# Performance work log

Hardware: AMD Instinct MI355X
Metric: run time of the kernel (lower is better)

## Reference

```python
import jax, jax.numpy as jnp
import numpy as np

EMA = 0.999
EPS = 1e-8


def setup_inputs() -> dict:
    key = jax.random.key(0)
    k1, k2, k3 = jax.random.split(key, 3)
    B, z_dim, H, W = 16, 64, 32, 32
    M = 4096
    N = B * H * W
    return {
        "z": jax.random.normal(k1, (B, z_dim, H, W), dtype=jnp.float32),
        "e": jax.random.normal(k2, (M, z_dim), dtype=jnp.float32),
        "belong": jax.random.uniform(k3, (N, M), dtype=jnp.float32),
        "log_sigma": jnp.zeros((1,), dtype=jnp.float32),
        "max_distance": jnp.ones((1, M), dtype=jnp.float32),
        "distance_p": 2,
    }


def reference(z, e, belong, log_sigma, max_distance, distance_p):
    B, z_dim, H, W = z.shape
    # [B, z_dim, H, W] -> [N, z_dim], N = B*H*W
    zf = jnp.transpose(z, (0, 2, 3, 1)).reshape(-1, z_dim)
    # pairwise L2 distance via GEMM expansion: ||z||^2 + ||e||^2 - 2 z.e
    d2 = (jnp.sum(zf * zf, axis=1, keepdims=True)
          + jnp.sum(e * e, axis=1)[None, :]
          - 2.0 * (zf @ e.T))                      # [N, M]
    distance = jnp.sqrt(jnp.maximum(d2, 0.0))
    # EMA update of per-code max distance (buffer, no grad in original)
    batch_max = jnp.max(belong * distance, axis=0, keepdims=True)  # [1, M]
    new_max = EMA * max_distance + (1.0 - EMA) * batch_max
    new_max = jax.lax.stop_gradient(jnp.clip(new_max, EPS, None))
    p = float(distance_p)
    distance = jnp.where(distance < new_max,
                         distance ** (2.0 / p),
                         distance ** (2.0 * p))
    alpha = -1.0 / (2.0 * jnp.exp(log_sigma) ** 2)  # shape (1,)
    lse = jax.scipy.special.logsumexp(alpha * distance, axis=0)  # [M]
    loss = -jnp.mean(lse) + z_dim * log_sigma  # shape (1,), as in torch
    return loss
```

## Files before the change

### kernel.cpp

```cpp
#include <hip/hip_runtime.h>
#include <hip/hip_bf16.h>

#define ZD   64
#define MM   4096
#define NN   16384
#define HWSZ 1024
#define BB   16

typedef __bf16 bf16x8 __attribute__((ext_vector_type(8)));
typedef float  f32x4  __attribute__((ext_vector_type(4)));

#define EMA_C 0.999f
#define EPS_C 1e-8f

__global__ __launch_bounds__(256) void k_prep(const float* __restrict__ z,
                                              const float* __restrict__ e,
                                              __hip_bfloat16* __restrict__ zf,
                                              __hip_bfloat16* __restrict__ ebf,
                                              float* __restrict__ zn2,
                                              float* __restrict__ en2,
                                              unsigned* __restrict__ bmax,
                                              unsigned* __restrict__ dmin,
                                              float* __restrict__ sume) {
    __shared__ float tile[64][65];
    __shared__ float part[4][64];
    int blk = blockIdx.x;
    int tid = threadIdx.x;
    if (blk < 256) {
        int b   = blk >> 4;
        int hw0 = (blk & 15) * 64;
        int tx = tid & 63, ty = tid >> 6;
        const float* zp = z + (size_t)b * (ZD * HWSZ);
#pragma unroll
        for (int kk = 0; kk < 16; kk++) {
            int k = kk * 4 + ty;
            tile[k][tx] = zp[(size_t)k * HWSZ + hw0 + tx];
        }
        __syncthreads();
#pragma unroll
        for (int i = 0; i < 16; i++) {
            int li = tid + i * 256;
            int ln = li >> 6, lk = li & 63;
            int n = b * HWSZ + hw0 + ln;
            zf[(size_t)n * ZD + lk] = __float2bfloat16(tile[lk][ln]);
        }
        float s = 0.f;
#pragma unroll
        for (int kk = 0; kk < 16; kk++) {
            float q = __bfloat162float(__float2bfloat16(tile[ty * 1 + kk * 4][tx]));
            s += q * q;
        }
        part[ty][tx] = s;
        __syncthreads();
        if (tid < 64) {
            float t = part[0][tid] + part[1][tid] + part[2][tid] + part[3][tid];
            zn2[b * HWSZ + hw0 + tid] = t;
        }
    } else {
        int eb  = blk - 256;
        int gid = eb * 256 + tid;
        if (gid < MM) {
            bmax[gid] = 0u;
            dmin[gid] = 0x7f800000u;
            sume[gid] = 0.f;
        }
        int wave = tid >> 6, lane = tid & 63;
        int row = eb * 4 + wave;
        if (row < MM) {
            float v = e[row * ZD + lane];
            __hip_bfloat16 b16 = __float2bfloat16(v);
            ebf[row * ZD + lane] = b16;
            float q = __bfloat162float(b16);
            float s = q * q;
            for (int off = 32; off; off >>= 1) s += __shfl_xor(s, off);
            if (lane == 0) en2[row] = s;
        }
    }
}

__device__ __forceinline__ void load_bl(const float* __restrict__ belong,
                                        int n0, int m0, int l16, int lq,
                                        f32x4 (&bl)[2][4]) {
#pragma unroll
    for (int im = 0; im < 2; im++)
#pragma unroll
        for (int jn = 0; jn < 4; jn++) {
            const f32x4* bp = reinterpret_cast<const f32x4*>(
                belong + (size_t)(n0 + jn * 16 + l16) * MM + (m0 + im * 16 + lq * 4));
            bl[im][jn] = __builtin_nontemporal_load(bp);
        }
}

__device__ __forceinline__ void p1_tile(const bf16x8* __restrict__ zfv,
                                        const float* __restrict__ zn2,
                                        int n0, int l16, int lq,
                                        const bf16x8 (&Af)[2][2],
                                        const f32x4 (&en2v)[2],
                                        const f32x4 (&bl)[2][4],
                                        float (&vmax2)[2][4],
                                        float (&vmin2)[2][4]) {
    bf16x8 Bf[4][2];
#pragma unroll
    for (int jn = 0; jn < 4; jn++)
#pragma unroll
        for (int h = 0; h < 2; h++)
            Bf[jn][h] = zfv[(size_t)(n0 + jn * 16 + l16) * 8 + h * 4 + lq];

    float zn2v[4];
#pragma unroll
    for (int jn = 0; jn < 4; jn++)
        zn2v[jn] = zn2[n0 + jn * 16 + l16];

    f32x4 acc[2][4];
#pragma unroll
    for (int im = 0; im < 2; im++)
#pragma unroll
        for (int jn = 0; jn < 4; jn++) {
            acc[im][jn] = (f32x4){0.f, 0.f, 0.f, 0.f};
            acc[im][jn] = __builtin_amdgcn_mfma_f32_16x16x32_bf16(Af[im][0], Bf[jn][0], acc[im][jn], 0, 0, 0);
            acc[im][jn] = __builtin_amdgcn_mfma_f32_16x16x32_bf16(Af[im][1], Bf[jn][1], acc[im][jn], 0, 0, 0);
        }

#pragma unroll
    for (int im = 0; im < 2; im++)
#pragma unroll
        for (int jn = 0; jn < 4; jn++)
#pragma unroll
            for (int r = 0; r < 4; r++) {
                float d2 = fmaxf(en2v[im][r] + zn2v[jn] - 2.f * acc[im][jn][r], 0.f);
                float b = bl[im][jn][r];
                vmax2[im][r] = fmaxf(vmax2[im][r], b * b * d2);
                vmin2[im][r] = fminf(vmin2[im][r], d2);
            }
}

__global__ __launch_bounds__(256, 2) void k_pass1(const __hip_bfloat16* __restrict__ zf,
                                                  const __hip_bfloat16* __restrict__ ebf,
                                                  const float* __restrict__ zn2,
                                                  const float* __restrict__ en2,
                                                  const float* __restrict__ belong,
                                                  unsigned* __restrict__ bmax,
                                                  unsigned* __restrict__ dmin) {
    int tid = threadIdx.x;
    int wave = tid >> 6, lane = tid & 63;
    int l16 = lane & 15, lq = lane >> 4;
    int wm = wave & 1, wn = wave >> 1;
    int m0 = blockIdx.x * 64 + wm * 32;
    int nbase = blockIdx.y * 1024 + wn * 64;

    const bf16x8* ebv = reinterpret_cast<const bf16x8*>(ebf);
    const bf16x8* zfv = reinterpret_cast<const bf16x8*>(zf);

    bf16x8 Af[2][2];
#pragma unroll
    for (int im = 0; im < 2; im++)
#pragma unroll
        for (int h = 0; h < 2; h++)
            Af[im][h] = ebv[(size_t)(m0 + im * 16 + l16) * 8 + h * 4 + lq];
    f32x4 en2v[2];
#pragma unroll
    for (int im = 0; im < 2; im++)
        en2v[im] = *reinterpret_cast<const f32x4*>(en2 + m0 + im * 16 + lq * 4);

    float vmax2[2][4], vmin2[2][4];
#pragma unroll
    for (int im = 0; im < 2; im++)
#pragma unroll
        for (int r = 0; r < 4; r++) { vmax2[im][r] = 0.f; vmin2[im][r] = 3.4e38f; }

    f32x4 blA[2][4], blB[2][4];
    load_bl(belong, nbase + 0 * 128, m0, l16, lq, blA);
    load_bl(belong, nbase + 1 * 128, m0, l16, lq, blB);

#pragma unroll 1
    for (int it = 0; it < 8; it += 2) {
        p1_tile(zfv, zn2, nbase + it * 128, l16, lq, Af, en2v, blA, vmax2, vmin2);
        if (it + 2 < 8) load_bl(belong, nbase + (it + 2) * 128, m0, l16, lq, blA);
        p1_tile(zfv, zn2, nbase + (it + 1) * 128, l16, lq, Af, en2v, blB, vmax2, vmin2);
        if (it + 3 < 8) load_bl(belong, nbase + (it + 3) * 128, m0, l16, lq, blB);
    }

#pragma unroll
    for (int off = 1; off < 16; off <<= 1)
#pragma unroll
        for (int im = 0; im < 2; im++)
#pragma unroll
            for (int r = 0; r < 4; r++) {
                vmax2[im][r] = fmaxf(vmax2[im][r], __shfl_xor(vmax2[im][r], off));
                vmin2[im][r] = fminf(vmin2[im][r], __shfl_xor(vmin2[im][r], off));
            }

    __shared__ unsigned smax[64], smin[64];
    if (tid < 64) { smax[tid] = 0u; smin[tid] = 0x7f800000u; }
    __syncthreads();
    if (l16 == 0) {
#pragma unroll
        for (int im = 0; im < 2; im++)
#pragma unroll
            for (int r = 0; r < 4; r++) {
                int ml = wm * 32 + im * 16 + lq * 4 + r;
                atomicMax(&smax[ml], __float_as_uint(sqrtf(vmax2[im][r])));
                atomicMin(&smin[ml], __float_as_uint(sqrtf(vmin2[im][r])));
            }
    }
    __syncthreads();
    if (tid < 64) {
        atomicMax(&bmax[blockIdx.x * 64 + tid], smax[tid]);
        atomicMin(&dmin[blockIdx.x * 64 + tid], smin[tid]);
    }
}

__global__ __launch_bounds__(256) void k_pass2(const __hip_bfloat16* __restrict__ zf,
                                               const __hip_bfloat16* __restrict__ ebf,
                                               const float* __restrict__ zn2,
                                               const float* __restrict__ en2,
                                               const unsigned* __restrict__ bmax,
                                               const unsigned* __restrict__ dmin,
                                               const float* __restrict__ max_distance,
                                               const float* __restrict__ log_sigma,
                                               const int* __restrict__ pp,
                                               float* __restrict__ refs,
                                               float* __restrict__ sume) {
    __shared__ float snm2[128], sref[128], ssum[128];
    int tid = threadIdx.x;
    int wave = tid >> 6, lane = tid & 63;
    int l16 = lane & 15, lq = lane >> 4;
    int wn = wave >> 1, wm = wave & 1;
    int m0 = blockIdx.y * 128 + wm * 64;

    int p = pp[0];
    float alpha = -0.5f * __expf(-2.f * log_sigma[0]);

    if (tid < 128) {
        int m = blockIdx.y * 128 + tid;
        float bm = __uint_as_float(bmax[m]);
        float dm = __uint_as_float(dmin[m]);
        float nm = fmaxf(EMA_C * max_distance[m] + (1.f - EMA_C) * bm, EPS_C);
        float tlow;
        if (p == 2) {
            float d4  = (dm * dm) * (dm * dm);
            float nm4 = (nm * nm) * (nm * nm);
            tlow = (dm < nm) ? fminf(dm, nm4) : d4;
        } else {
            float e1 = 2.f / (float)p, e2 = 2.f * (float)p;
            tlow = (dm < nm) ? fminf(powf(dm, e1), powf(nm, e2)) : powf(dm, e2);
        }
        float rf = alpha * tlow;
        snm2[tid] = nm * nm;
        sref[tid] = rf;
        ssum[tid] = 0.f;
        if (blockIdx.x == 0) refs[m] = rf;
    }
    __syncthreads();

    const bf16x8* zfv = reinterpret_cast<const bf16x8*>(zf);
    const bf16x8* ebv = reinterpret_cast<const bf16x8*>(ebf);

    bf16x8 Bf[4][2];
#pragma unroll
    for (int j = 0; j < 4; j++)
#pragma unroll
        for (int h = 0; h < 2; h++)
            Bf[j][h] = ebv[(size_t)(m0 + j * 16 + l16) * 8 + h * 4 + lq];
    float en2s[4], nm2s[4], rfs[4];
#pragma unroll
    for (int j = 0; j < 4; j++) {
        en2s[j] = en2[m0 + j * 16 + l16];
        nm2s[j] = snm2[wm * 64 + j * 16 + l16];
        rfs[j]  = sref[wm * 64 + j * 16 + l16];
    }

    bool p2 = (p == 2);
    float pe = (float)p, pi = 1.f / (float)p;

    float csum[4] = {0.f, 0.f, 0.f, 0.f};

#pragma unroll 1
    for (int it = 0; it < 4; it++) {
        int n0 = blockIdx.x * 256 + it * 64 + wn * 32;

        bf16x8 Af[2][2];
#pragma unroll
        for (int i = 0; i < 2; i++)
#pragma unroll
            for (int h = 0; h < 2; h++)
                Af[i][h] = zfv[(size_t)(n0 + i * 16 + l16) * 8 + h * 4 + lq];

        f32x4 acc[2][4];
#pragma unroll
        for (int i = 0; i < 2; i++)
#pragma unroll
            for (int j = 0; j < 4; j++) {
                acc[i][j] = (f32x4){0.f, 0.f, 0.f, 0.f};
                acc[i][j] = __builtin_amdgcn_mfma_f32_16x16x32_bf16(Af[i][0], Bf[j][0], acc[i][j], 0, 0, 0);
                acc[i][j] = __builtin_amdgcn_mfma_f32_16x16x32_bf16(Af[i][1], Bf[j][1], acc[i][j], 0, 0, 0);
            }

        f32x4 zn2v[2];
#pragma unroll
        for (int i = 0; i < 2; i++)
            zn2v[i] = *reinterpret_cast<const f32x4*>(zn2 + n0 + i * 16 + lq * 4);

#pragma unroll
        for (int j = 0; j < 4; j++) {
            float en2v = en2s[j];
            float nm2v = nm2s[j];
            float rfv  = rfs[j];
#pragma unroll
            for (int i = 0; i < 2; i++)
#pragma unroll
                for (int r = 0; r < 4; r++) {
                    float d2c = fmaxf(zn2v[i][r] + en2v - 2.f * acc[i][j][r], 0.f);
                    float t;
                    if (p2) t = (d2c < nm2v) ? sqrtf(d2c) : d2c * d2c;
                    else    t = powf(d2c, (d2c < nm2v) ? pi : pe);
                    csum[j] += __expf(fmaf(alpha, t, -rfv));
                }
        }
    }

#pragma unroll
    for (int j = 0; j < 4; j++) {
        csum[j] += __shfl_xor(csum[j], 16);
        csum[j] += __shfl_xor(csum[j], 32);
        if (lane < 16) atomicAdd(&ssum[wm * 64 + j * 16 + lane], csum[j]);
    }
    __syncthreads();
    if (tid < 128) atomicAdd(&sume[blockIdx.y * 128 + tid], ssum[tid]);
}

__global__ __launch_bounds__(256) void k_final(const float* __restrict__ refs,
                                               const float* __restrict__ sume,
                                               const float* __restrict__ log_sigma,
                                               float* __restrict__ out) {
    __shared__ float red[4];
    int tid = threadIdx.x;
    float a = 0.f;
    for (int m = tid; m < MM; m += 256)
        a += refs[m] + logf(fmaxf(sume[m], 1e-30f));
    for (int off = 32; off; off >>= 1) a += __shfl_xor(a, off);
    int wave = tid >> 6, lane = tid & 63;
    if (lane == 0) red[wave] = a;
    __syncthreads();
    if (tid == 0) {
        float t = red[0] + red[1] + red[2] + red[3];
        out[0] = -t / (float)MM + (float)ZD * log_sigma[0];
    }
}

extern "C" void kernel_launch(void* const* d_in, const int* in_sizes, int n_in,
                              void* d_out, int out_size, void* d_ws, size_t ws_size,
                              hipStream_t stream) {
    const float* z            = (const float*)d_in[0];
    const float* e            = (const float*)d_in[1];
    const float* belong       = (const float*)d_in[2];
    const float* log_sigma    = (const float*)d_in[3];
    const float* max_distance = (const float*)d_in[4];
    const int*   pp           = (const int*)d_in[5];
    float* out = (float*)d_out;

    char* ws = (char*)d_ws;
    __hip_bfloat16* zf  = (__hip_bfloat16*)(ws + 0);
    __hip_bfloat16* ebf = (__hip_bfloat16*)(ws + 2097152);
    float*    zn2  = (float*)(ws + 2621440);
    float*    en2  = (float*)(ws + 2686976);
    unsigned* bmax = (unsigned*)(ws + 2703360);
    unsigned* dmin = (unsigned*)(ws + 2719744);
    float*    refs = (float*)(ws + 2736128);
    float*    sume = (float*)(ws + 2752512);

    k_prep<<<1280, 256, 0, stream>>>(z, e, zf, ebf, zn2, en2, bmax, dmin, sume);
    k_pass1<<<dim3(MM / 64, NN / 1024), 256, 0, stream>>>(zf, ebf, zn2, en2, belong, bmax, dmin);
    k_pass2<<<dim3(NN / 256, MM / 128), 256, 0, stream>>>(zf, ebf, zn2, en2, bmax, dmin,
                                                          max_distance, log_sigma, pp, refs, sume);
    k_final<<<1, 256, 0, stream>>>(refs, sume, log_sigma, out);
}
```

Measured before the change: 449.7 us.

## Fuse final reduction into pass2 via last-block counter and enlarge pass2 tiles

Removes the separate k_final launch. The last pass2 block, detected with an atomic done counter plus thread fences, recomputes the per-code reference terms and does the log-sum reduction itself. Each pass2 block now covers 1024 rows instead of 256, so there are 4x fewer blocks and fewer per-block setup steps and sume atomics. The trade-off is less grid parallelism (512 blocks) and a serialized tail in the last block.

```diff
diff --git a/kernel.cpp b/kernel.cpp
--- a/kernel.cpp
+++ b/kernel.cpp
@@ -6,6 +6,8 @@
 #define NN   16384
 #define HWSZ 1024
 #define BB   16
+
+#define NBLK2 512
 
 typedef __bf16 bf16x8 __attribute__((ext_vector_type(8)));
 typedef float  f32x4  __attribute__((ext_vector_type(4)));
@@ -21,7 +23,8 @@
                                               float* __restrict__ en2,
                                               unsigned* __restrict__ bmax,
                                               unsigned* __restrict__ dmin,
-                                              float* __restrict__ sume) {
+                                              float* __restrict__ sume,
+                                              unsigned* __restrict__ done) {
     __shared__ float tile[64][65];
     __shared__ float part[4][64];
     int blk = blockIdx.x;
@@ -64,6 +67,7 @@
             dmin[gid] = 0x7f800000u;
             sume[gid] = 0.f;
         }
+        if (gid == 0) done[0] = 0u;
         int wave = tid >> 6, lane = tid & 63;
         int row = eb * 4 + wave;
         if (row < MM) {
@@ -210,6 +214,20 @@
     }
 }
 
+__device__ __forceinline__ float ref_of(float bm, float dm, float md, int p, float alpha) {
+    float nm = fmaxf(EMA_C * md + (1.f - EMA_C) * bm, EPS_C);
+    float tlow;
+    if (p == 2) {
+        float d4  = (dm * dm) * (dm * dm);
+        float nm4 = (nm * nm) * (nm * nm);
+        tlow = (dm < nm) ? fminf(dm, nm4) : d4;
+    } else {
+        float e1 = 2.f / (float)p, e2 = 2.f * (float)p;
+        tlow = (dm < nm) ? fminf(powf(dm, e1), powf(nm, e2)) : powf(dm, e2);
+    }
+    return alpha * tlow;
+}
+
 __global__ __launch_bounds__(256) void k_pass2(const __hip_bfloat16* __restrict__ zf,
                                                const __hip_bfloat16* __restrict__ ebf,
                                                const float* __restrict__ zn2,
@@ -219,9 +237,12 @@
                                                const float* __restrict__ max_distance,
                                                const float* __restrict__ log_sigma,
                                                const int* __restrict__ pp,
-                                               float* __restrict__ refs,
-                                               float* __restrict__ sume) {
+                                               float* __restrict__ sume,
+                                               unsigned* __restrict__ done,
+                                               float* __restrict__ out) {
     __shared__ float snm2[128], sref[128], ssum[128];
+    __shared__ unsigned lastflag;
+    __shared__ float red[4];
     int tid = threadIdx.x;
     int wave = tid >> 6, lane = tid & 63;
     int l16 = lane & 15, lq = lane >> 4;
@@ -236,20 +257,9 @@
         float bm = __uint_as_float(bmax[m]);
         float dm = __uint_as_float(dmin[m]);
         float nm = fmaxf(EMA_C * max_distance[m] + (1.f - EMA_C) * bm, EPS_C);
-        float tlow;
-        if (p == 2) {
-            float d4  = (dm * dm) * (dm * dm);
-            float nm4 = (nm * nm) * (nm * nm);
-            tlow = (dm < nm) ? fminf(dm, nm4) : d4;
-        } else {
-            float e1 = 2.f / (float)p, e2 = 2.f * (float)p;
-            tlow = (dm < nm) ? fminf(powf(dm, e1), powf(nm, e2)) : powf(dm, e2);
-        }
-        float rf = alpha * tlow;
         snm2[tid] = nm * nm;
-        sref[tid] = rf;
+        sref[tid] = ref_of(bm, dm, max_distance[m], p, alpha);
         ssum[tid] = 0.f;
-        if (blockIdx.x == 0) refs[m] = rf;
     }
     __syncthreads();
 
@@ -276,8 +286,8 @@
     float csum[4] = {0.f, 0.f, 0.f, 0.f};
 
 #pragma unroll 1
-    for (int it = 0; it < 4; it++) {
-        int n0 = blockIdx.x * 256 + it * 64 + wn * 32;
+    for (int it = 0; it < 16; it++) {
+        int n0 = blockIdx.x * 1024 + it * 64 + wn * 32;
 
         bf16x8 Af[2][2];
 #pragma unroll
@@ -327,24 +337,31 @@
     }
     __syncthreads();
     if (tid < 128) atomicAdd(&sume[blockIdx.y * 128 + tid], ssum[tid]);
-}
-
-__global__ __launch_bounds__(256) void k_final(const float* __restrict__ refs,
-                                               const float* __restrict__ sume,
-                                               const float* __restrict__ log_sigma,
-                                               float* __restrict__ out) {
-    __shared__ float red[4];
-    int tid = threadIdx.x;
-    float a = 0.f;
-    for (int m = tid; m < MM; m += 256)
-        a += refs[m] + logf(fmaxf(sume[m], 1e-30f));
-    for (int off = 32; off; off >>= 1) a += __shfl_xor(a, off);
-    int wave = tid >> 6, lane = tid & 63;
-    if (lane == 0) red[wave] = a;
-    __syncthreads();
+
+    __threadfence();
     if (tid == 0) {
-        float t = red[0] + red[1] + red[2] + red[3];
-        out[0] = -t / (float)MM + (float)ZD * log_sigma[0];
+        unsigned prev = atomicAdd(done, 1u);
+        lastflag = (prev == NBLK2 - 1) ? 1u : 0u;
+    }
+    __syncthreads();
+    if (lastflag) {
+        __threadfence();
+        float a = 0.f;
+        for (int m = tid; m < MM; m += 256) {
+            float bm = __uint_as_float(bmax[m]);
+            float dm = __uint_as_float(dmin[m]);
+            float rf = ref_of(bm, dm, max_distance[m], p, alpha);
+            float s = __hip_atomic_load(&sume[m], __ATOMIC_RELAXED,
+                                        __HIP_MEMORY_SCOPE_AGENT);
+            a += rf + logf(fmaxf(s, 1e-30f));
+        }
+        for (int off = 32; off; off >>= 1) a += __shfl_xor(a, off);
+        if (lane == 0) red[wave] = a;
+        __syncthreads();
+        if (tid == 0) {
+            float t = red[0] + red[1] + red[2] + red[3];
+            out[0] = -t / (float)MM + (float)ZD * log_sigma[0];
+        }
     }
 }
 
@@ -366,12 +383,12 @@
     float*    en2  = (float*)(ws + 2686976);
     unsigned* bmax = (unsigned*)(ws + 2703360);
     unsigned* dmin = (unsigned*)(ws + 2719744);
-    float*    refs = (float*)(ws + 2736128);
+    unsigned* done = (unsigned*)(ws + 2736128);
     float*    sume = (float*)(ws + 2752512);
 
-    k_prep<<<1280, 256, 0, stream>>>(z, e, zf, ebf, zn2, en2, bmax, dmin, sume);
+    k_prep<<<1280, 256, 0, stream>>>(z, e, zf, ebf, zn2, en2, bmax, dmin, sume, done);
     k_pass1<<<dim3(MM / 64, NN / 1024), 256, 0, stream>>>(zf, ebf, zn2, en2, belong, bmax, dmin);
-    k_pass2<<<dim3(NN / 256, MM / 128), 256, 0, stream>>>(zf, ebf, zn2, en2, bmax, dmin,
-                                                          max_distance, log_sigma, pp, refs, sume);
-    k_final<<<1, 256, 0, stream>>>(refs, sume, log_sigma, out);
-}
+    k_pass2<<<dim3(NN / 1024, MM / 128), 256, 0, stream>>>(zf, ebf, zn2, en2, bmax, dmin,
+                                                           max_distance, log_sigma, pp,
+                                                           sume, done, out);
+}
```

Result: slower. 477.9 us (+6.3%).
